# Kernel optimization log

Hardware: AMD Instinct MI355X
Metric: run time of the kernel (lower is better)

## Reference

```python
import jax, jax.numpy as jnp
import numpy as np

B, S, H = 2, 1024, 2048          # batch, seq, hidden
NH, HD = 32, 64                  # heads, head_dim
E, M, K = 8, 1024, 2             # experts, moe_dim, top_k
EPS = 1e-5
ROPE_THETA = 10000.0


def setup_inputs() -> dict:
    key = jax.random.key(0)
    ks = jax.random.split(key, 12)
    sc = lambda *sh: 0.02
    return {
        "hidden_states": jax.random.normal(ks[0], (B, S, H), jnp.float32),
        "w_attn_norm": jnp.ones((H,), jnp.float32),
        "Wq": jax.random.normal(ks[1], (H, H), jnp.float32) * 0.02,
        "Wk": jax.random.normal(ks[2], (H, H), jnp.float32) * 0.02,
        "Wv": jax.random.normal(ks[3], (H, H), jnp.float32) * 0.02,
        "Wo": jax.random.normal(ks[4], (H, H), jnp.float32) * 0.02,
        "w_moe_norm": jnp.ones((H,), jnp.float32),
        "Wr": jax.random.normal(ks[5], (H, E), jnp.float32) * 0.02,
        "Wgate": jax.random.normal(ks[6], (E, H, M), jnp.float32) * 0.02,
        "Wup": jax.random.normal(ks[7], (E, H, M), jnp.float32) * 0.02,
        "Wdown": jax.random.normal(ks[8], (E, M, H), jnp.float32) * 0.02,
    }


def _rmsnorm(x, w):
    return x * jax.lax.rsqrt(jnp.mean(x * x, axis=-1, keepdims=True) + EPS) * w


def _rope_cos_sin(seq_len, dtype):
    inv_freq = 1.0 / (ROPE_THETA ** (jnp.arange(0, HD, 2, dtype=jnp.float32) / HD))
    ang = jnp.arange(seq_len, dtype=jnp.float32)[:, None] * inv_freq[None, :]  # [S, HD/2]
    cos = jnp.concatenate([jnp.cos(ang), jnp.cos(ang)], axis=-1).astype(dtype)  # [S, HD]
    sin = jnp.concatenate([jnp.sin(ang), jnp.sin(ang)], axis=-1).astype(dtype)
    return cos, sin


def _rotate_half(x):
    x1, x2 = jnp.split(x, 2, axis=-1)
    return jnp.concatenate([-x2, x1], axis=-1)


def _attention(x, Wq, Wk, Wv, Wo, mask):
    b, s, _ = x.shape
    def heads(t):  # [b,s,H] -> [b,NH,s,HD]
        return t.reshape(b, s, NH, HD).transpose(0, 2, 1, 3)
    q, k, v = heads(x @ Wq), heads(x @ Wk), heads(x @ Wv)
    cos, sin = _rope_cos_sin(s, x.dtype)
    q = q * cos + _rotate_half(q) * sin
    k = k * cos + _rotate_half(k) * sin
    scores = jnp.einsum("bhqd,bhkd->bhqk", q, k) / jnp.sqrt(jnp.asarray(HD, x.dtype))
    scores = scores + mask  # [1,1,s,s] causal
    attn = jax.nn.softmax(scores, axis=-1)
    out = jnp.einsum("bhqk,bhkd->bhqd", attn, v)
    out = out.transpose(0, 2, 1, 3).reshape(b, s, H)
    return out @ Wo


def _moe(x, Wr, Wgate, Wup, Wdown):
    b, s, _ = x.shape
    xf = x.reshape(b * s, H)  # [T, H]
    logits = xf @ Wr  # [T, E]
    probs = jax.nn.softmax(logits, axis=-1)
    topv, topi = jax.lax.top_k(probs, K)  # [T, K]
    topv = topv / jnp.sum(topv, axis=-1, keepdims=True)
    # combine weights [T, E], zero for unselected experts
    cw = jnp.sum(jax.nn.one_hot(topi, E, dtype=xf.dtype) * topv[..., None], axis=1)
    g = jnp.einsum("th,ehm->etm", xf, Wgate)
    u = jnp.einsum("th,ehm->etm", xf, Wup)
    h = jax.nn.silu(g) * u
    expert_out = jnp.einsum("etm,emh->eth", h, Wdown)  # [E, T, H]
    out = jnp.einsum("eth,te->th", expert_out, cw)
    return out.reshape(b, s, H)


def reference(hidden_states, w_attn_norm, Wq, Wk, Wv, Wo, w_moe_norm, Wr, Wgate, Wup, Wdown):
    b, s, _ = hidden_states.shape
    causal = jnp.triu(jnp.full((s, s), -jnp.inf, hidden_states.dtype), k=1)[None, None]
    residual = hidden_states
    x = _rmsnorm(hidden_states, w_attn_norm)
    x = _attention(x, Wq, Wk, Wv, Wo, causal)
    x = x + residual
    residual = x
    y = _rmsnorm(x, w_moe_norm)
    y = _moe(y, Wr, Wgate, Wup, Wdown)
    return y + residual
```

## Files before the change

kernel.cpp:

```cpp
#include <hip/hip_runtime.h>
#include <hip/hip_bf16.h>
#include <cstdint>

typedef unsigned short u16;
typedef __bf16 bf16x4_t __attribute__((ext_vector_type(4)));
typedef __bf16 bf16x8_t __attribute__((ext_vector_type(8)));
typedef float f32x4_t __attribute__((ext_vector_type(4)));
typedef unsigned short us4_t __attribute__((ext_vector_type(4)));
typedef unsigned short us8_t __attribute__((ext_vector_type(8)));

#define BATCH 2
#define SEQ 1024
#define HID 2048
#define NHEAD 32
#define NEXP 8
#define MDIM 1024
#define T_TOK (BATCH*SEQ)


__device__ __forceinline__ void gload16(const void* g, void* l){
  __builtin_amdgcn_global_load_lds((__attribute__((address_space(1))) void*)(uintptr_t)g,
                                   (__attribute__((address_space(3))) void*)l, 16, 0, 0);
}

__device__ __forceinline__ bf16x8_t ldfsw64(const u16* base, int row, int colbyte){
  const char* p = (const char*)base + row*64;
  int sw = (row & 3) << 4;
  bf16x4_t a = *(const bf16x4_t*)(p + (colbyte ^ sw));
  bf16x4_t b = *(const bf16x4_t*)(p + ((colbyte + 32) ^ sw));
  return __builtin_shufflevector(a, b, 0,1,2,3,4,5,6,7);
}

__device__ __forceinline__ f32x4_t mfma16(bf16x8_t a, bf16x8_t b, f32x4_t c){
  return __builtin_amdgcn_mfma_f32_16x16x32_bf16(a, b, c, 0, 0, 0);
}

__device__ __forceinline__ u16 f2b(float f){
  __hip_bfloat16 h = __float2bfloat16(f);
  return __builtin_bit_cast(u16, h);
}
__device__ __forceinline__ float b2f(u16 b){
  return __builtin_bit_cast(float, (unsigned int)b << 16);
}
__device__ __forceinline__ void split3v(float v, u16& b1, u16& b2, u16& b3){
  b1 = f2b(v); float f1 = b2f(b1);
  float r1 = v - f1;
  b2 = f2b(r1); float f2 = b2f(b2);
  b3 = f2b(r1 - f2);
}



__global__ __launch_bounds__(256)
void convT_fl(const float* __restrict__ in, u16* __restrict__ out, int R, int C)
{
  __shared__ float t[64][65];
  const int KB = C >> 5;
  int bz = blockIdx.z;
  const float* ip = in + (size_t)bz * R * C;
  u16* op = out + (size_t)bz * R * C;
  int r0 = blockIdx.y*64, c0 = blockIdx.x*64;
  int tid = threadIdx.x;
  int lr = tid >> 4;
  int lc = (tid & 15) * 4;
  #pragma unroll
  for (int i = 0; i < 4; i++){
    int r = lr + i*16;
    float4 v = *(const float4*)&ip[(size_t)(r0 + r) * R + c0 + lc];
    t[r][lc] = v.x; t[r][lc+1] = v.y; t[r][lc+2] = v.z; t[r][lc+3] = v.w;
  }
  __syncthreads();
  if (tid < 128){
    int n_l = tid & 63;
    int kb2 = tid >> 6;
    int gn = c0 + n_l;
    int rb = gn >> 7, sub = (gn >> 4) & 7, frn = gn & 15;
    int kb = (r0 >> 5) + kb2;
    size_t fo = (((size_t)(rb*KB + kb)*8 + sub)*64 + frn*4) * 8;
    #pragma unroll
    for (int fg = 0; fg < 4; fg++){
      us8_t w;
      #pragma unroll
      for (int j = 0; j < 4; j++){
        w[j]   = f2b(t[kb2*32 + fg*4 + j][n_l]);
        w[j+4] = f2b(t[kb2*32 + fg*4 + 16 + j][n_l]);
      }
      *(us8_t*)&op[fo + fg*8] = w;
    }
  }
}


__global__ __launch_bounds__(256)
void convT3(const float* __restrict__ in, u16* __restrict__ o1, u16* __restrict__ o2,
            u16* __restrict__ o3)
{
  __shared__ float t[64][65];
  int r0 = blockIdx.y*64, c0 = blockIdx.x*64;
  int tid = threadIdx.x;
  int lr = tid >> 4;
  int lc = (tid & 15) * 4;
  #pragma unroll
  for (int i = 0; i < 4; i++){
    int r = lr + i*16;
    float4 v = *(const float4*)&in[(size_t)(r0 + r) * HID + c0 + lc];
    t[r][lc] = v.x; t[r][lc+1] = v.y; t[r][lc+2] = v.z; t[r][lc+3] = v.w;
  }
  __syncthreads();
  if (tid < 128){
    int n  = tid & 63;
    int kb2 = tid >> 6;
    int gn = c0 + n;
    int nb = gn >> 7, sub = (gn >> 4) & 7, fr = gn & 15;
    int kb = (r0 >> 5) + kb2;
    size_t fo = (((size_t)(nb*64 + kb)*8 + sub)*64 + fr*4) * 8;
    #pragma unroll
    for (int fg = 0; fg < 4; fg++){
      us8_t w1, w2, w3;
      #pragma unroll
      for (int j = 0; j < 4; j++){
        u16 b1, b2, b3;
        split3v(t[kb2*32 + fg*4 + j][n], b1, b2, b3);
        w1[j] = b1; w2[j] = b2; w3[j] = b3;
        split3v(t[kb2*32 + fg*4 + 16 + j][n], b1, b2, b3);
        w1[j+4] = b1; w2[j+4] = b2; w3[j+4] = b3;
      }
      *(us8_t*)&o1[fo + fg*8] = w1;
      *(us8_t*)&o2[fo + fg*8] = w2;
      *(us8_t*)&o3[fo + fg*8] = w3;
    }
  }
}


__global__ __launch_bounds__(256)
void rmsnorm3_k(const float* __restrict__ x, const float* __restrict__ w,
                u16* __restrict__ o1, u16* __restrict__ o2, u16* __restrict__ o3)
{
  int row = blockIdx.x;
  const float* xr = x + (size_t)row * HID;
  int tid = threadIdx.x;
  int kb = tid >> 2, fg = tid & 3;
  int kbase = kb*32 + fg*4;
  float4 a = *(const float4*)(xr + kbase);
  float4 b = *(const float4*)(xr + kbase + 16);
  float ss = a.x*a.x + a.y*a.y + a.z*a.z + a.w*a.w
           + b.x*b.x + b.y*b.y + b.z*b.z + b.w*b.w;
  #pragma unroll
  for (int off = 32; off; off >>= 1) ss += __shfl_down(ss, off);
  __shared__ float red[4];
  if ((tid & 63) == 0) red[tid >> 6] = ss;
  __syncthreads();
  float tot = red[0] + red[1] + red[2] + red[3];
  float rs = (float)(1.0 / sqrt((double)tot * (1.0/2048.0) + 1e-5));
  float4 wa = *(const float4*)(w + kbase);
  float4 wb = *(const float4*)(w + kbase + 16);
  float o[8];
  o[0]=a.x*rs*wa.x; o[1]=a.y*rs*wa.y; o[2]=a.z*rs*wa.z; o[3]=a.w*rs*wa.w;
  o[4]=b.x*rs*wb.x; o[5]=b.y*rs*wb.y; o[6]=b.z*rs*wb.z; o[7]=b.w*rs*wb.w;
  us8_t w1, w2, w3;
  #pragma unroll
  for (int j = 0; j < 8; j++){
    u16 b1, b2, b3; split3v(o[j], b1, b2, b3);
    w1[j] = b1; w2[j] = b2; w3[j] = b3;
  }
  int rb = row >> 7, sub = (row >> 4) & 7, fr = row & 15;
  size_t fo = (((size_t)(rb*64 + kb)*8 + sub)*64 + fr*4 + fg) * 8;
  *(us8_t*)&o1[fo] = w1; *(us8_t*)&o2[fo] = w2; *(us8_t*)&o3[fo] = w3;
}


__global__ __launch_bounds__(256)
void rmsnorm_k(const float* __restrict__ x, const float* __restrict__ w,
               u16* __restrict__ ob, float* __restrict__ of, float* __restrict__ oi)
{
  int row = blockIdx.x;
  const float* xr = x + (size_t)row * HID;
  int base = threadIdx.x * 8;
  float4 a = *(const float4*)(xr + base);
  float4 b = *(const float4*)(xr + base + 4);
  float ss = a.x*a.x + a.y*a.y + a.z*a.z + a.w*a.w
           + b.x*b.x + b.y*b.y + b.z*b.z + b.w*b.w;
  #pragma unroll
  for (int off = 32; off; off >>= 1) ss += __shfl_down(ss, off);
  __shared__ float red[4];
  if ((threadIdx.x & 63) == 0) red[threadIdx.x >> 6] = ss;
  __syncthreads();
  float tot = red[0] + red[1] + red[2] + red[3];
  float rs = (float)(1.0 / sqrt((double)tot * (1.0/2048.0) + 1e-5));
  float4 wa = *(const float4*)(w + base);
  float4 wb = *(const float4*)(w + base + 4);
  float o[8];
  o[0]=a.x*rs*wa.x; o[1]=a.y*rs*wa.y; o[2]=a.z*rs*wa.z; o[3]=a.w*rs*wa.w;
  o[4]=b.x*rs*wb.x; o[5]=b.y*rs*wb.y; o[6]=b.z*rs*wb.z; o[7]=b.w*rs*wb.w;
  us4_t p0, p1;
  p0.x=f2b(o[0]); p0.y=f2b(o[1]); p0.z=f2b(o[2]); p0.w=f2b(o[3]);
  p1.x=f2b(o[4]); p1.y=f2b(o[5]); p1.z=f2b(o[6]); p1.w=f2b(o[7]);
  *(us4_t*)&ob[(size_t)row*HID + base] = p0;
  *(us4_t*)&ob[(size_t)row*HID + base + 4] = p1;
  float* orow = of + (size_t)row*HID + base;
  *(float4*)orow = make_float4(o[0],o[1],o[2],o[3]);
  *(float4*)(orow+4) = make_float4(o[4],o[5],o[6],o[7]);
  float* irow = oi + (size_t)row*HID + base;
  *(float4*)irow = a;
  *(float4*)(irow+4) = b;
}


__global__ void rope_table_k(float* ct, float* st){
  int i = blockIdx.x*256 + threadIdx.x;
  int s = i >> 5, j = i & 31;
  double invf = exp(-(double)j / 32.0 * log(10000.0));
  double ang = (double)s * invf;
  ct[i] = (float)cos(ang);
  st[i] = (float)sin(ang);
}


__global__ __launch_bounds__(256, 2)
void gemm_qkv(const u16* __restrict__ A1, const u16* __restrict__ A2, const u16* __restrict__ A3,
              const u16* __restrict__ Wq1, const u16* __restrict__ Wq2, const u16* __restrict__ Wq3,
              const u16* __restrict__ Wk1, const u16* __restrict__ Wk2, const u16* __restrict__ Wk3,
              const u16* __restrict__ Wv1, const u16* __restrict__ Wv2, const u16* __restrict__ Wv3,
              u16* __restrict__ oq1, u16* __restrict__ oq2, u16* __restrict__ oq3,
              u16* __restrict__ ok1, u16* __restrict__ ok2, u16* __restrict__ ok3,
              float* __restrict__ vf,
              const float* __restrict__ ct, const float* __restrict__ st)
{
  __shared__ u16 As[3][128*32];
  __shared__ u16 Bs[3][128*32];
  const int flat = blockIdx.x + 16*blockIdx.y + 256*blockIdx.z;
  const int logical = (flat & 7) * 96 + (flat >> 3);
  const int z  = logical >> 8;
  const int bm = ((logical >> 4) & 15) * 128;
  const int bn = (logical & 15) * 128;
  const int tid = threadIdx.x;
  const int lane = tid & 63;
  const int wave = tid >> 6;
  const int wr = wave >> 1, wc = wave & 1;
  const int fr = lane & 15, fg = lane >> 4;

  f32x4_t acc[4][4] = {};

  const u16* Ap[3] = {A1, A2, A3};
  const u16* Bp[3];
  if (z == 0)      { Bp[0] = Wq1; Bp[1] = Wq2; Bp[2] = Wq3; }
  else if (z == 1) { Bp[0] = Wk1; Bp[1] = Wk2; Bp[2] = Wk3; }
  else             { Bp[0] = Wv1; Bp[1] = Wv2; Bp[2] = Wv3; }
  const u16* gA[3]; const u16* gB[3];
  #pragma unroll
  for (int t = 0; t < 3; t++){
    gA[t] = Ap[t] + (size_t)(bm >> 7) * 64 * 4096 + tid*8;
    gB[t] = Bp[t] + (size_t)(bn >> 7) * 64 * 4096 + tid*8;
  }

  for (int kb = 0; kb < 64; kb++){
    const size_t o = (size_t)kb * 4096;
    #pragma unroll
    for (int t = 0; t < 3; t++){
      gload16(gA[t] + o,        &As[t][tid*8]);
      gload16(gA[t] + o + 2048, &As[t][2048 + tid*8]);
      gload16(gB[t] + o,        &Bs[t][tid*8]);
      gload16(gB[t] + o + 2048, &Bs[t][2048 + tid*8]);
    }
    __syncthreads();
    bf16x8_t bfv[3][4];
    #pragma unroll
    for (int t = 0; t < 3; t++)
      #pragma unroll
      for (int ni = 0; ni < 4; ni++)
        bfv[t][ni] = *(const bf16x8_t*)&Bs[t][(((wc*4 + ni)*64) + fr*4 + fg)*8];
    #pragma unroll
    for (int mi = 0; mi < 4; mi++){
      const int ao = (((wr*4 + mi)*64) + fr*4 + fg)*8;
      bf16x8_t a1 = *(const bf16x8_t*)&As[0][ao];
      bf16x8_t a2 = *(const bf16x8_t*)&As[1][ao];
      bf16x8_t a3 = *(const bf16x8_t*)&As[2][ao];
      #pragma unroll
      for (int ni = 0; ni < 4; ni++){
        f32x4_t c = acc[mi][ni];
        c = mfma16(a3, bfv[0][ni], c);
        c = mfma16(a2, bfv[1][ni], c);
        c = mfma16(a1, bfv[2][ni], c);
        c = mfma16(a2, bfv[0][ni], c);
        c = mfma16(a1, bfv[1][ni], c);
        c = mfma16(a1, bfv[0][ni], c);
        acc[mi][ni] = c;
      }
    }
    __syncthreads();
  }

  if (z < 2){
    u16* O1 = z ? ok1 : oq1;
    u16* O2 = z ? ok2 : oq2;
    u16* O3 = z ? ok3 : oq3;
    const int h = (bn + wc*64) >> 6;
    #pragma unroll
    for (int mi = 0; mi < 4; mi++)
      #pragma unroll
      for (int r = 0; r < 4; r++){
        int row = bm + wr*64 + mi*16 + fg*4 + r;
        int s = row & (SEQ-1);
        int b = row >> 10;
        int tok = row & 1023;
        int tb = tok >> 4;
        int frk = fg*4 + r;
        size_t sb = (size_t)(b*NHEAD + h) * 65536;
        #pragma unroll
        for (int ni = 0; ni < 2; ni++){
          int dlo = ni*16 + fr;
          float c  = ct[s*32 + dlo];
          float sn = st[s*32 + dlo];
          float xl = acc[mi][ni][r], xh = acc[mi][ni+2][r];
          float ol = xl*c - xh*sn;
          float oh = xh*c + xl*sn;
          size_t a0 = sb + ((size_t)(tb*2 + 0)*64 + frk*4 + (fr>>2))*8 + ni*4 + (fr&3);
          size_t a1 = sb + ((size_t)(tb*2 + 1)*64 + frk*4 + (fr>>2))*8 + ni*4 + (fr&3);
          u16 b1, b2, b3;
          split3v(ol, b1, b2, b3); O1[a0] = b1; O2[a0] = b2; O3[a0] = b3;
          split3v(oh, b1, b2, b3); O1[a1] = b1; O2[a1] = b2; O3[a1] = b3;
        }
      }
  } else {
    #pragma unroll
    for (int mi = 0; mi < 4; mi++)
      #pragma unroll
      for (int ni = 0; ni < 4; ni++)
        #pragma unroll
        for (int r = 0; r < 4; r++){
          int row = bm + wr*64 + mi*16 + fg*4 + r;
          int col = bn + wc*64 + ni*16 + fr;
          vf[(size_t)row * HID + col] = acc[mi][ni][r];
        }
  }
}


__global__ __launch_bounds__(256, 2)
void gemm_o(const u16* __restrict__ A1, const u16* __restrict__ A2, const u16* __restrict__ A3,
            const u16* __restrict__ B1, const u16* __restrict__ B2, const u16* __restrict__ B3,
            float* __restrict__ Cf, const float* __restrict__ Res)
{
  __shared__ u16 As[3][128*32];
  __shared__ u16 Bs[3][64*32];
  const int flat = blockIdx.x + 32*blockIdx.y;
  const int logical = (flat & 7) * 64 + (flat >> 3);
  const int bn = (logical & 31) * 64;
  const int bm = (logical >> 5) * 128;
  const int tid = threadIdx.x;
  const int lane = tid & 63;
  const int wave = tid >> 6;
  const int wr = wave >> 1, wc = wave & 1;
  const int fr = lane & 15, fg = lane >> 4;

  f32x4_t acc[4][2] = {};

  const u16* Ap[3] = {A1, A2, A3};
  const u16* Bp[3] = {B1, B2, B3};
  const u16* gA[3]; const u16* gB[3];
  const int sb0 = (bn >> 4) & 7;
  #pragma unroll
  for (int t = 0; t < 3; t++){
    gA[t] = Ap[t] + (size_t)(bm >> 7) * 64 * 4096 + tid*8;
    gB[t] = Bp[t] + (size_t)(bn >> 7) * 64 * 4096 + sb0*512 + tid*8;
  }

  for (int kb = 0; kb < 64; kb++){
    const size_t o = (size_t)kb * 4096;
    #pragma unroll
    for (int t = 0; t < 3; t++){
      gload16(gA[t] + o,        &As[t][tid*8]);
      gload16(gA[t] + o + 2048, &As[t][2048 + tid*8]);
      gload16(gB[t] + o,        &Bs[t][tid*8]);
    }
    __syncthreads();
    bf16x8_t bfv[3][2];
    #pragma unroll
    for (int t = 0; t < 3; t++)
      #pragma unroll
      for (int nj = 0; nj < 2; nj++)
        bfv[t][nj] = *(const bf16x8_t*)&Bs[t][(((wc*2 + nj)*64) + fr*4 + fg)*8];
    #pragma unroll
    for (int mi = 0; mi < 4; mi++){
      const int ao = (((wr*4 + mi)*64) + fr*4 + fg)*8;
      bf16x8_t a1 = *(const bf16x8_t*)&As[0][ao];
      bf16x8_t a2 = *(const bf16x8_t*)&As[1][ao];
      bf16x8_t a3 = *(const bf16x8_t*)&As[2][ao];
      #pragma unroll
      for (int nj = 0; nj < 2; nj++){
        f32x4_t c = acc[mi][nj];
        c = mfma16(a3, bfv[0][nj], c);
        c = mfma16(a2, bfv[1][nj], c);
        c = mfma16(a1, bfv[2][nj], c);
        c = mfma16(a2, bfv[0][nj], c);
        c = mfma16(a1, bfv[1][nj], c);
        c = mfma16(a1, bfv[0][nj], c);
        acc[mi][nj] = c;
      }
    }
    __syncthreads();
  }

  #pragma unroll
  for (int mi = 0; mi < 4; mi++)
    #pragma unroll
    for (int nj = 0; nj < 2; nj++)
      #pragma unroll
      for (int r = 0; r < 4; r++){
        int row = bm + wr*64 + mi*16 + fg*4 + r;
        int col = bn + wc*32 + nj*16 + fr;
        size_t idx = (size_t)row * HID + col;
        Cf[idx] = acc[mi][nj][r] + Res[idx];
      }
}


__global__ __launch_bounds__(256)
void vtrans3_k(const float* __restrict__ vf, u16* __restrict__ t1, u16* __restrict__ t2,
               u16* __restrict__ t3)
{
  __shared__ float t[64][65];
  int st0 = blockIdx.x * 64;
  int bh = blockIdx.y;
  int b = bh >> 5, h = bh & 31;
  int tid = threadIdx.x;
  #pragma unroll
  for (int i = 0; i < 4; i++){
    int idx = tid + i*256;
    int s = idx >> 4, dc = (idx & 15) * 4;
    float4 v = *(const float4*)&vf[(size_t)(b*SEQ + st0 + s) * HID + h*64 + dc];
    t[dc+0][s] = v.x; t[dc+1][s] = v.y; t[dc+2][s] = v.z; t[dc+3][s] = v.w;
  }
  __syncthreads();
  #pragma unroll
  for (int it = 0; it < 2; it++){
    int rho = tid + it*256;
    int kbv_l = rho >> 8;
    int db    = (rho >> 6) & 3;
    int lane  = rho & 63;
    int d = db*16 + (lane >> 2);
    int fgv = lane & 3;
    us8_t w1, w2, w3;
    #pragma unroll
    for (int j = 0; j < 8; j++){
      int half = j >> 2, e = j & 3;
      int tokl = kbv_l*32 + half*16 + fgv*4 + e;
      u16 b1, b2, b3; split3v(t[d][tokl], b1, b2, b3);
      w1[j] = b1; w2[j] = b2; w3[j] = b3;
    }
    size_t base = (size_t)bh*65536 + ((size_t)(((st0>>5) + kbv_l)*4 + db)*64 + lane)*8;
    *(us8_t*)&t1[base] = w1; *(us8_t*)&t2[base] = w2; *(us8_t*)&t3[base] = w3;
  }
}


__global__ __launch_bounds__(256)
void fattn3_k(const u16* __restrict__ q1, const u16* __restrict__ q2, const u16* __restrict__ q3,
              const u16* __restrict__ k1, const u16* __restrict__ k2, const u16* __restrict__ k3,
              const u16* __restrict__ v1, const u16* __restrict__ v2, const u16* __restrict__ v3,
              u16* __restrict__ ao1, u16* __restrict__ ao2, u16* __restrict__ ao3)
{
  __shared__ u16 Ks[3][4096];
  __shared__ u16 Vs[3][4096];
  __shared__ u16 Ps[2][4][1024];
  const int bh = blockIdx.x, qt = blockIdx.y;
  const int b = bh >> 5, h = bh & 31;
  const int tid = threadIdx.x, lane = tid & 63, wave = tid >> 6;
  const int fr = lane & 15, fg = lane >> 4;
  const size_t hslab = (size_t)bh * 65536;

  bf16x8_t aq[3][2];
  {
    size_t qo = hslab + (size_t)(qt*4 + wave)*1024 + (size_t)(fr*4 + fg)*8;
    aq[0][0] = *(const bf16x8_t*)&q1[qo]; aq[0][1] = *(const bf16x8_t*)&q1[qo + 512];
    aq[1][0] = *(const bf16x8_t*)&q2[qo]; aq[1][1] = *(const bf16x8_t*)&q2[qo + 512];
    aq[2][0] = *(const bf16x8_t*)&q3[qo]; aq[2][1] = *(const bf16x8_t*)&q3[qo + 512];
  }

  f32x4_t oacc[4] = {};
  float m_r[4], l_r[4];
  #pragma unroll
  for (int r = 0; r < 4; r++){ m_r[r] = -1e30f; l_r[r] = 0.f; }

  const u16* kp[3] = { k1 + hslab, k2 + hslab, k3 + hslab };
  const u16* vp[3] = { v1 + hslab, v2 + hslab, v3 + hslab };

  for (int kt = 0; kt <= qt; kt++){
    const size_t o = (size_t)kt * 4096;
    #pragma unroll
    for (int t = 0; t < 3; t++){
      gload16(kp[t] + o + tid*8,        &Ks[t][tid*8]);
      gload16(kp[t] + o + 2048 + tid*8, &Ks[t][2048 + tid*8]);
      gload16(vp[t] + o + tid*8,        &Vs[t][tid*8]);
      gload16(vp[t] + o + 2048 + tid*8, &Vs[t][2048 + tid*8]);
    }
    __syncthreads();

    f32x4_t sc[4] = {};
    #pragma unroll
    for (int nf = 0; nf < 4; nf++)
      #pragma unroll
      for (int ks = 0; ks < 2; ks++){
        const int ko = ((nf*2 + ks)*64 + fr*4 + fg)*8;
        bf16x8_t bk0 = *(const bf16x8_t*)&Ks[0][ko];
        bf16x8_t bk1 = *(const bf16x8_t*)&Ks[1][ko];
        bf16x8_t bk2 = *(const bf16x8_t*)&Ks[2][ko];
        sc[nf] = mfma16(aq[2][ks], bk0, sc[nf]);
        sc[nf] = mfma16(aq[1][ks], bk1, sc[nf]);
        sc[nf] = mfma16(aq[0][ks], bk2, sc[nf]);
        sc[nf] = mfma16(aq[1][ks], bk0, sc[nf]);
        sc[nf] = mfma16(aq[0][ks], bk1, sc[nf]);
        sc[nf] = mfma16(aq[0][ks], bk0, sc[nf]);
      }

    float nm[4] = {-1e30f,-1e30f,-1e30f,-1e30f};
    #pragma unroll
    for (int nf = 0; nf < 4; nf++)
      #pragma unroll
      for (int r = 0; r < 4; r++){
        float v = sc[nf][r] * 0.125f;
        if (kt == qt && nf*16 + fr > wave*16 + fg*4 + r) v = -1e30f;
        sc[nf][r] = v;
        nm[r] = fmaxf(nm[r], v);
      }
    #pragma unroll
    for (int r = 0; r < 4; r++)
      #pragma unroll
      for (int msk = 8; msk; msk >>= 1) nm[r] = fmaxf(nm[r], __shfl_xor(nm[r], msk));

    #pragma unroll
    for (int r = 0; r < 4; r++){
      float mn = fmaxf(m_r[r], nm[r]);
      float f = __expf(m_r[r] - mn);
      m_r[r] = mn;
      float rsum = 0.f;
      #pragma unroll
      for (int nf = 0; nf < 4; nf++){
        float pv = __expf(sc[nf][r] - mn);
        sc[nf][r] = pv;
        rsum += pv;
      }
      #pragma unroll
      for (int msk = 8; msk; msk >>= 1) rsum += __shfl_xor(rsum, msk);
      l_r[r] = l_r[r]*f + rsum;
      #pragma unroll
      for (int df = 0; df < 4; df++) oacc[df][r] *= f;
    }

    #pragma unroll
    for (int nf = 0; nf < 4; nf++)
      #pragma unroll
      for (int r = 0; r < 4; r++){
        float pv = sc[nf][r];
        u16 b1 = f2b(pv);
        float f1 = b2f(b1);
        u16 b2 = f2b(pv - f1);
        int pa = ((nf>>1)*64 + (fg*4 + r)*4 + (fr>>2))*8 + (nf&1)*4 + (fr&3);
        Ps[0][wave][pa] = b1;
        Ps[1][wave][pa] = b2;
      }

    #pragma unroll
    for (int ks = 0; ks < 2; ks++){
      bf16x8_t pa0 = *(const bf16x8_t*)&Ps[0][wave][(ks*64 + fr*4 + fg)*8];
      bf16x8_t pa1 = *(const bf16x8_t*)&Ps[1][wave][(ks*64 + fr*4 + fg)*8];
      #pragma unroll
      for (int df = 0; df < 4; df++){
        const int vo = ((ks*4 + df)*64 + fr*4 + fg)*8;
        bf16x8_t bv0 = *(const bf16x8_t*)&Vs[0][vo];
        bf16x8_t bv1 = *(const bf16x8_t*)&Vs[1][vo];
        bf16x8_t bv2 = *(const bf16x8_t*)&Vs[2][vo];
        oacc[df] = mfma16(pa0, bv2, oacc[df]);
        oacc[df] = mfma16(pa1, bv1, oacc[df]);
        oacc[df] = mfma16(pa1, bv0, oacc[df]);
        oacc[df] = mfma16(pa0, bv1, oacc[df]);
        oacc[df] = mfma16(pa0, bv0, oacc[df]);
      }
    }
    __syncthreads();
  }

  #pragma unroll
  for (int r = 0; r < 4; r++){
    float inv = 1.f / l_r[r];
    int orow = b*SEQ + qt*64 + wave*16 + fg*4 + r;
    int rb = orow >> 7, sub = (orow >> 4) & 7, frA = orow & 15;
    #pragma unroll
    for (int df = 0; df < 4; df++){
      float val = oacc[df][r] * inv;
      int kb = h*2 + (df >> 1);
      size_t addr = ((((size_t)rb*64 + kb)*8 + sub)*64 + frA*4 + (fr>>2))*8 + (df&1)*4 + (fr&3);
      u16 b1, b2, b3; split3v(val, b1, b2, b3);
      ao1[addr] = b1; ao2[addr] = b2; ao3[addr] = b3;
    }
  }
}


__global__ __launch_bounds__(64)
void router_scatter_k(const float* __restrict__ yn, const float* __restrict__ Wr,
                      int* __restrict__ tok_list, float* __restrict__ w_list,
                      int* __restrict__ cur){
  int row = blockIdx.x;
  int lane = threadIdx.x;
  const float* xr = yn + (size_t)row * HID;
  double acc[8] = {};
  for (int j = lane; j < HID; j += 64){
    double xv = (double)xr[j];
    const float* wr = Wr + (size_t)j*8;
    float4 w0 = *(const float4*)wr;
    float4 w1 = *(const float4*)(wr + 4);
    acc[0] += xv*w0.x; acc[1] += xv*w0.y; acc[2] += xv*w0.z; acc[3] += xv*w0.w;
    acc[4] += xv*w1.x; acc[5] += xv*w1.y; acc[6] += xv*w1.z; acc[7] += xv*w1.w;
  }
  #pragma unroll
  for (int e = 0; e < 8; e++)
    #pragma unroll
    for (int off = 32; off; off >>= 1) acc[e] += __shfl_down(acc[e], off);
  if (lane == 0){
    double mx = acc[0];
    #pragma unroll
    for (int e = 1; e < 8; e++) mx = fmax(mx, acc[e]);
    double p[8];
    #pragma unroll
    for (int e = 0; e < 8; e++) p[e] = exp(acc[e] - mx);
    int i1 = 0;
    #pragma unroll
    for (int e = 1; e < 8; e++) if (p[e] > p[i1]) i1 = e;
    int i2 = (i1 == 0) ? 1 : 0;
    #pragma unroll
    for (int e = 0; e < 8; e++) if (e != i1 && p[e] > p[i2]) i2 = e;
    double s2 = p[i1] + p[i2];
    int pos1 = atomicAdd(&cur[i1], 1);
    tok_list[i1*T_TOK + pos1] = row;
    w_list[i1*T_TOK + pos1] = (float)(p[i1] / s2);
    int pos2 = atomicAdd(&cur[i2], 1);
    tok_list[i2*T_TOK + pos2] = row;
    w_list[i2*T_TOK + pos2] = (float)(p[i2] / s2);
  }
}

__global__ __launch_bounds__(128)
void pad_k(const int* __restrict__ cur, int* __restrict__ tok_list,
           float* __restrict__ w_list, int* __restrict__ cnt_pad){
  int e = blockIdx.x;
  int c = cur[e];
  int cp = (c + 127) & ~127;
  for (int i = c + threadIdx.x; i < cp; i += 128){
    tok_list[e*T_TOK + i] = 0;
    w_list[e*T_TOK + i] = 0.f;
  }
  if (threadIdx.x == 0) cnt_pad[e] = cp;
}


__global__ __launch_bounds__(256, 2)
void gemm_gateup_sp(const u16* __restrict__ A, const u16* __restrict__ WgT, const u16* __restrict__ WuT,
                    const int* __restrict__ tok_list, const float* __restrict__ w_list,
                    const int* __restrict__ cnt_pad, u16* __restrict__ Hb)
{
  const int e = blockIdx.z;
  const int bm = blockIdx.y * 128;
  if (bm >= cnt_pad[e]) return;
  __shared__ u16 As[128*32];
  __shared__ u16 Bg[64*32];
  __shared__ u16 Bu[64*32];
  const int tid = threadIdx.x;
  const int lane = tid & 63;
  const int wave = tid >> 6;
  const int wr = wave >> 1, wc = wave & 1;
  const int fr = lane & 15, fg = lane >> 4;
  const int bn = blockIdx.x * 64;

  f32x4_t ag[4][2] = {}, au[4][2] = {};

  const int srow = tid >> 2, skb = (tid & 3) ^ (srow & 3);
  const int tok0 = tok_list[e*T_TOK + bm + srow];
  const int tok1 = tok_list[e*T_TOK + bm + srow + 64];
  const u16* ga0 = A + (size_t)tok0 * HID + skb * 8;
  const u16* ga1 = A + (size_t)tok1 * HID + skb * 8;
  const int sub0 = (bn >> 4) & 7;
  const u16* gg = WgT + (size_t)e*MDIM*HID + ((size_t)(bn>>7)*512 + sub0)*512 + tid*8;
  const u16* gu = WuT + (size_t)e*MDIM*HID + ((size_t)(bn>>7)*512 + sub0)*512 + tid*8;

  for (int kb = 0; kb < 64; kb++){
    gload16(ga0 + kb*32, &As[tid*8]);
    gload16(ga1 + kb*32, &As[2048 + tid*8]);
    gload16(gg + (size_t)kb*4096, &Bg[tid*8]);
    gload16(gu + (size_t)kb*4096, &Bu[tid*8]);
    __syncthreads();
    bf16x8_t af[4], bg[2], bu[2];
    #pragma unroll
    for (int i = 0; i < 4; i++) af[i] = ldfsw64(As, wr*64 + i*16 + fr, fg*8);
    #pragma unroll
    for (int j = 0; j < 2; j++){
      bg[j] = *(const bf16x8_t*)&Bg[((wc*2 + j)*64 + fr*4 + fg)*8];
      bu[j] = *(const bf16x8_t*)&Bu[((wc*2 + j)*64 + fr*4 + fg)*8];
    }
    #pragma unroll
    for (int mi = 0; mi < 4; mi++)
      #pragma unroll
      for (int nj = 0; nj < 2; nj++){
        ag[mi][nj] = mfma16(af[mi], bg[nj], ag[mi][nj]);
        au[mi][nj] = mfma16(af[mi], bu[nj], au[mi][nj]);
      }
    __syncthreads();
  }

  #pragma unroll
  for (int mi = 0; mi < 4; mi++)
    #pragma unroll
    for (int nj = 0; nj < 2; nj++)
      #pragma unroll
      for (int r = 0; r < 4; r++){
        int pos = bm + wr*64 + mi*16 + fg*4 + r;
        int col = bn + wc*32 + nj*16 + fr;
        float g = ag[mi][nj][r], u = au[mi][nj][r];
        float h = g / (1.0f + __expf(-g)) * u * w_list[e*T_TOK + pos];
        Hb[((size_t)e*T_TOK + pos)*MDIM + col] = f2b(h);
      }
}


__global__ __launch_bounds__(256, 2)
void gemm_down_sp(const u16* __restrict__ Hb, const u16* __restrict__ WdT,
                  const int* __restrict__ tok_list, const int* __restrict__ cnt_pad,
                  float* __restrict__ Out)
{
  const int e = blockIdx.z;
  const int bm = blockIdx.y * 128;
  if (bm >= cnt_pad[e]) return;
  __shared__ u16 As[128*32];
  __shared__ u16 Bs[128*32];
  const int tid = threadIdx.x;
  const int lane = tid & 63;
  const int wave = tid >> 6;
  const int wr = wave >> 1, wc = wave & 1;
  const int fr = lane & 15, fg = lane >> 4;
  const int bn = blockIdx.x * 128;
  const int srow = tid >> 2, skb = (tid & 3) ^ (srow & 3);

  f32x4_t acc[4][4] = {};

  const u16* A  = Hb  + (size_t)e * T_TOK * MDIM;
  const u16* ga0 = A + (size_t)(bm + srow) * MDIM + skb * 8;
  const u16* gB = WdT + (size_t)e*HID*MDIM + (size_t)(bn>>7)*131072 + tid*8;
  for (int kb = 0; kb < 32; kb++){
    gload16(ga0 + kb*32, &As[tid*8]);
    gload16(ga0 + (size_t)64*MDIM + kb*32, &As[2048 + tid*8]);
    gload16(gB + (size_t)kb*4096,        &Bs[tid*8]);
    gload16(gB + (size_t)kb*4096 + 2048, &Bs[2048 + tid*8]);
    __syncthreads();
    bf16x8_t af[4], bfv[4];
    #pragma unroll
    for (int i = 0; i < 4; i++) af[i]  = ldfsw64(As, wr*64 + i*16 + fr, fg*8);
    #pragma unroll
    for (int i = 0; i < 4; i++) bfv[i] = *(const bf16x8_t*)&Bs[((wc*4 + i)*64 + fr*4 + fg)*8];
    #pragma unroll
    for (int mi = 0; mi < 4; mi++)
      #pragma unroll
      for (int ni = 0; ni < 4; ni++)
        acc[mi][ni] = mfma16(af[mi], bfv[ni], acc[mi][ni]);
    __syncthreads();
  }

  #pragma unroll
  for (int mi = 0; mi < 4; mi++)
    #pragma unroll
    for (int r = 0; r < 4; r++){
      int pos = bm + wr*64 + mi*16 + fg*4 + r;
      int tok = tok_list[e*T_TOK + pos];
      #pragma unroll
      for (int ni = 0; ni < 4; ni++){
        int col = bn + wc*64 + ni*16 + fr;
        atomicAdd(&Out[(size_t)tok * HID + col], acc[mi][ni][r]);
      }
    }
}


extern "C" void kernel_launch(void* const* d_in, const int* in_sizes, int n_in,
                              void* d_out, int out_size, void* d_ws, size_t ws_size,
                              hipStream_t stream)
{
  const float* hs     = (const float*)d_in[0];
  const float* w_attn = (const float*)d_in[1];
  const float* Wq = (const float*)d_in[2];
  const float* Wk = (const float*)d_in[3];
  const float* Wv = (const float*)d_in[4];
  const float* Wo = (const float*)d_in[5];
  const float* w_moe = (const float*)d_in[6];
  const float* Wr = (const float*)d_in[7];
  const float* Wg = (const float*)d_in[8];
  const float* Wu = (const float*)d_in[9];
  const float* Wd = (const float*)d_in[10];
  float* out = (float*)d_out;
  (void)in_sizes; (void)n_in; (void)out_size; (void)ws_size;

  char* ws = (char*)d_ws;
  const size_t MB = 1024*1024;
  char* R0 = ws;
  char* R1 = ws + 96*MB;
  char* R2 = ws + 120*MB;
  char* R3 = ws + 144*MB;
  char* R4 = ws + 168*MB;
  char* R5 = ws + 184*MB;
  char* RS = ws + 208*MB;

  const size_t WSLB = (size_t)HID*HID;
  u16* W0 = (u16*)R0;
  u16 *Wq1 = W0,          *Wq2 = W0 + WSLB,    *Wq3 = W0 + 2*WSLB;
  u16 *Wk1 = W0 + 3*WSLB, *Wk2 = W0 + 4*WSLB,  *Wk3 = W0 + 5*WSLB;
  u16 *Wv1 = W0 + 6*WSLB, *Wv2 = W0 + 7*WSLB,  *Wv3 = W0 + 8*WSLB;
  u16 *Wo1 = W0 + 9*WSLB, *Wo2 = W0 + 10*WSLB, *Wo3 = W0 + 11*WSLB;
  const size_t TSLB = (size_t)T_TOK*HID;
  u16 *xn1 = (u16*)R1, *xn2 = (u16*)R1 + TSLB, *xn3 = (u16*)R1 + 2*TSLB;
  u16 *q1  = (u16*)R2, *q2  = (u16*)R2 + TSLB, *q3  = (u16*)R2 + 2*TSLB;
  u16 *k1  = (u16*)R3, *k2  = (u16*)R3 + TSLB, *k3  = (u16*)R3 + 2*TSLB;
  u16 *vt1 = xn1, *vt2 = xn2, *vt3 = xn3;
  float* vf  = (float*)R4;
  float* x1  = (float*)R4;
  u16 *ao1 = (u16*)R5, *ao2 = (u16*)R5 + TSLB, *ao3 = (u16*)R5 + 2*TSLB;
  u16* WgT = (u16*)R0;
  u16* WuT = (u16*)R0 + (size_t)NEXP*MDIM*HID;
  u16* WdT = (u16*)R0 + 2*(size_t)NEXP*MDIM*HID;
  u16* ynb = (u16*)R1;
  float* yn = (float*)(R1 + 8*MB);
  u16* hb  = (u16*)R2;
  int*   tok_list = (int*)RS;
  float* w_list   = (float*)(RS + 64*1024);
  int*   cur      = (int*)(RS + 128*1024);
  int*   cnt_pad  = (int*)(RS + 132*1024);
  float* ct   = (float*)(RS + 256*1024);
  float* stab = (float*)(RS + 384*1024);

  dim3 blk256(256), gMoE(16,16,8);

  rope_table_k<<<dim3(SEQ*32/256), blk256, 0, stream>>>(ct, stab);
  convT3<<<dim3(HID/64, HID/64), blk256, 0, stream>>>(Wq, Wq1, Wq2, Wq3);
  convT3<<<dim3(HID/64, HID/64), blk256, 0, stream>>>(Wk, Wk1, Wk2, Wk3);
  convT3<<<dim3(HID/64, HID/64), blk256, 0, stream>>>(Wv, Wv1, Wv2, Wv3);
  convT3<<<dim3(HID/64, HID/64), blk256, 0, stream>>>(Wo, Wo1, Wo2, Wo3);

  rmsnorm3_k<<<dim3(T_TOK), blk256, 0, stream>>>(hs, w_attn, xn1, xn2, xn3);

  gemm_qkv<<<dim3(16,16,3), blk256, 0, stream>>>(xn1,xn2,xn3,
      Wq1,Wq2,Wq3, Wk1,Wk2,Wk3, Wv1,Wv2,Wv3,
      q1,q2,q3, k1,k2,k3, vf, ct, stab);

  vtrans3_k<<<dim3(SEQ/64, BATCH*NHEAD), blk256, 0, stream>>>(vf, vt1, vt2, vt3);

  fattn3_k<<<dim3(BATCH*NHEAD, SEQ/64), blk256, 0, stream>>>(q1,q2,q3, k1,k2,k3,
      vt1,vt2,vt3, ao1,ao2,ao3);

  gemm_o<<<dim3(32,16), blk256, 0, stream>>>(ao1,ao2,ao3, Wo1,Wo2,Wo3, x1, hs);

  convT_fl<<<dim3(MDIM/64, HID/64, NEXP), blk256, 0, stream>>>(Wg, WgT, MDIM, HID);
  convT_fl<<<dim3(MDIM/64, HID/64, NEXP), blk256, 0, stream>>>(Wu, WuT, MDIM, HID);
  convT_fl<<<dim3(HID/64, MDIM/64, NEXP), blk256, 0, stream>>>(Wd, WdT, HID, MDIM);

  rmsnorm_k<<<dim3(T_TOK), blk256, 0, stream>>>(x1, w_moe, ynb, yn, out);

  hipMemsetAsync(cur, 0, NEXP*sizeof(int), stream);
  router_scatter_k<<<dim3(T_TOK), dim3(64), 0, stream>>>(yn, Wr, tok_list, w_list, cur);
  pad_k<<<dim3(NEXP), dim3(128), 0, stream>>>(cur, tok_list, w_list, cnt_pad);

  gemm_gateup_sp<<<gMoE, blk256, 0, stream>>>(ynb, WgT, WuT, tok_list, w_list, cnt_pad, hb);
  gemm_down_sp<<<gMoE, blk256, 0, stream>>>(hb, WdT, tok_list, cnt_pad, out);
}
```

Baseline: 843.8 us.

## Load B operands directly from global into registers, dropping LDS staging

In the QKV, O-projection, MoE gate/up and down GEMMs and the flash-attention kernel, the pre-fragmented weight/K/V tiles are now read straight from global memory into registers in MFMA fragment layout instead of being staged through shared memory. This frees LDS so the launch bounds are raised to allow three blocks per CU, and the attention kernel loses its per-tile barriers. The trade-off is that each wave now fetches B fragments independently, so waves sharing a column slice read the same data twice and L2/global traffic rises. Load latency is also no longer hidden behind an LDS barrier.

```diff
diff --git a/kernel.cpp b/kernel.cpp
--- a/kernel.cpp
+++ b/kernel.cpp
@@ -217,7 +217,7 @@
 }
 
 
-__global__ __launch_bounds__(256, 2)
+__global__ __launch_bounds__(256, 3)
 void gemm_qkv(const u16* __restrict__ A1, const u16* __restrict__ A2, const u16* __restrict__ A3,
               const u16* __restrict__ Wq1, const u16* __restrict__ Wq2, const u16* __restrict__ Wq3,
               const u16* __restrict__ Wk1, const u16* __restrict__ Wk2, const u16* __restrict__ Wk3,
@@ -228,7 +228,6 @@
               const float* __restrict__ ct, const float* __restrict__ st)
 {
   __shared__ u16 As[3][128*32];
-  __shared__ u16 Bs[3][128*32];
   const int flat = blockIdx.x + 16*blockIdx.y + 256*blockIdx.z;
   const int logical = (flat & 7) * 96 + (flat >> 3);
   const int z  = logical >> 8;
@@ -247,11 +246,11 @@
   if (z == 0)      { Bp[0] = Wq1; Bp[1] = Wq2; Bp[2] = Wq3; }
   else if (z == 1) { Bp[0] = Wk1; Bp[1] = Wk2; Bp[2] = Wk3; }
   else             { Bp[0] = Wv1; Bp[1] = Wv2; Bp[2] = Wv3; }
-  const u16* gA[3]; const u16* gB[3];
+  const u16* gA[3]; const u16* gBf[3];
   #pragma unroll
   for (int t = 0; t < 3; t++){
-    gA[t] = Ap[t] + (size_t)(bm >> 7) * 64 * 4096 + tid*8;
-    gB[t] = Bp[t] + (size_t)(bn >> 7) * 64 * 4096 + tid*8;
+    gA[t]  = Ap[t] + (size_t)(bm >> 7) * 262144 + tid*8;
+    gBf[t] = Bp[t] + (size_t)(bn >> 7) * 262144 + ((wc*4)*64 + fr*4 + fg)*8;
   }
 
   for (int kb = 0; kb < 64; kb++){
@@ -260,16 +259,14 @@
     for (int t = 0; t < 3; t++){
       gload16(gA[t] + o,        &As[t][tid*8]);
       gload16(gA[t] + o + 2048, &As[t][2048 + tid*8]);
-      gload16(gB[t] + o,        &Bs[t][tid*8]);
-      gload16(gB[t] + o + 2048, &Bs[t][2048 + tid*8]);
-    }
+    }
+    bf16x8_t bfv[3][4];
+    #pragma unroll
+    for (int t = 0; t < 3; t++)
+      #pragma unroll
+      for (int ni = 0; ni < 4; ni++)
+        bfv[t][ni] = *(const bf16x8_t*)(gBf[t] + o + ni*512);
     __syncthreads();
-    bf16x8_t bfv[3][4];
-    #pragma unroll
-    for (int t = 0; t < 3; t++)
-      #pragma unroll
-      for (int ni = 0; ni < 4; ni++)
-        bfv[t][ni] = *(const bf16x8_t*)&Bs[t][(((wc*4 + ni)*64) + fr*4 + fg)*8];
     #pragma unroll
     for (int mi = 0; mi < 4; mi++){
       const int ao = (((wr*4 + mi)*64) + fr*4 + fg)*8;
@@ -343,7 +340,6 @@
             float* __restrict__ Cf, const float* __restrict__ Res)
 {
   __shared__ u16 As[3][128*32];
-  __shared__ u16 Bs[3][64*32];
   const int flat = blockIdx.x + 32*blockIdx.y;
   const int logical = (flat & 7) * 64 + (flat >> 3);
   const int bn = (logical & 31) * 64;
@@ -358,12 +354,12 @@
 
   const u16* Ap[3] = {A1, A2, A3};
   const u16* Bp[3] = {B1, B2, B3};
-  const u16* gA[3]; const u16* gB[3];
+  const u16* gA[3]; const u16* gBf[3];
   const int sb0 = (bn >> 4) & 7;
   #pragma unroll
   for (int t = 0; t < 3; t++){
-    gA[t] = Ap[t] + (size_t)(bm >> 7) * 64 * 4096 + tid*8;
-    gB[t] = Bp[t] + (size_t)(bn >> 7) * 64 * 4096 + sb0*512 + tid*8;
+    gA[t]  = Ap[t] + (size_t)(bm >> 7) * 262144 + tid*8;
+    gBf[t] = Bp[t] + (size_t)(bn >> 7) * 262144 + (size_t)(sb0 + wc*2)*512 + (fr*4 + fg)*8;
   }
 
   for (int kb = 0; kb < 64; kb++){
@@ -372,15 +368,14 @@
     for (int t = 0; t < 3; t++){
       gload16(gA[t] + o,        &As[t][tid*8]);
       gload16(gA[t] + o + 2048, &As[t][2048 + tid*8]);
-      gload16(gB[t] + o,        &Bs[t][tid*8]);
-    }
+    }
+    bf16x8_t bfv[3][2];
+    #pragma unroll
+    for (int t = 0; t < 3; t++)
+      #pragma unroll
+      for (int nj = 0; nj < 2; nj++)
+        bfv[t][nj] = *(const bf16x8_t*)(gBf[t] + o + nj*512);
     __syncthreads();
-    bf16x8_t bfv[3][2];
-    #pragma unroll
-    for (int t = 0; t < 3; t++)
-      #pragma unroll
-      for (int nj = 0; nj < 2; nj++)
-        bfv[t][nj] = *(const bf16x8_t*)&Bs[t][(((wc*2 + nj)*64) + fr*4 + fg)*8];
     #pragma unroll
     for (int mi = 0; mi < 4; mi++){
       const int ao = (((wr*4 + mi)*64) + fr*4 + fg)*8;
@@ -455,14 +450,12 @@
 }
 
 
-__global__ __launch_bounds__(256)
+__global__ __launch_bounds__(256, 3)
 void fattn3_k(const u16* __restrict__ q1, const u16* __restrict__ q2, const u16* __restrict__ q3,
               const u16* __restrict__ k1, const u16* __restrict__ k2, const u16* __restrict__ k3,
               const u16* __restrict__ v1, const u16* __restrict__ v2, const u16* __restrict__ v3,
               u16* __restrict__ ao1, u16* __restrict__ ao2, u16* __restrict__ ao3)
 {
-  __shared__ u16 Ks[3][4096];
-  __shared__ u16 Vs[3][4096];
   __shared__ u16 Ps[2][4][1024];
   const int bh = blockIdx.x, qt = blockIdx.y;
   const int b = bh >> 5, h = bh & 31;
@@ -483,29 +476,22 @@
   #pragma unroll
   for (int r = 0; r < 4; r++){ m_r[r] = -1e30f; l_r[r] = 0.f; }
 
-  const u16* kp[3] = { k1 + hslab, k2 + hslab, k3 + hslab };
-  const u16* vp[3] = { v1 + hslab, v2 + hslab, v3 + hslab };
+  const int fo = (fr*4 + fg)*8;
+  const u16* kf[3] = { k1 + hslab + fo, k2 + hslab + fo, k3 + hslab + fo };
+  const u16* vfp[3] = { v1 + hslab + fo, v2 + hslab + fo, v3 + hslab + fo };
 
   for (int kt = 0; kt <= qt; kt++){
     const size_t o = (size_t)kt * 4096;
-    #pragma unroll
-    for (int t = 0; t < 3; t++){
-      gload16(kp[t] + o + tid*8,        &Ks[t][tid*8]);
-      gload16(kp[t] + o + 2048 + tid*8, &Ks[t][2048 + tid*8]);
-      gload16(vp[t] + o + tid*8,        &Vs[t][tid*8]);
-      gload16(vp[t] + o + 2048 + tid*8, &Vs[t][2048 + tid*8]);
-    }
-    __syncthreads();
 
     f32x4_t sc[4] = {};
     #pragma unroll
     for (int nf = 0; nf < 4; nf++)
       #pragma unroll
       for (int ks = 0; ks < 2; ks++){
-        const int ko = ((nf*2 + ks)*64 + fr*4 + fg)*8;
-        bf16x8_t bk0 = *(const bf16x8_t*)&Ks[0][ko];
-        bf16x8_t bk1 = *(const bf16x8_t*)&Ks[1][ko];
-        bf16x8_t bk2 = *(const bf16x8_t*)&Ks[2][ko];
+        const size_t ko = o + (nf*2 + ks)*512;
+        bf16x8_t bk0 = *(const bf16x8_t*)(kf[0] + ko);
+        bf16x8_t bk1 = *(const bf16x8_t*)(kf[1] + ko);
+        bf16x8_t bk2 = *(const bf16x8_t*)(kf[2] + ko);
         sc[nf] = mfma16(aq[2][ks], bk0, sc[nf]);
         sc[nf] = mfma16(aq[1][ks], bk1, sc[nf]);
         sc[nf] = mfma16(aq[0][ks], bk2, sc[nf]);
@@ -567,10 +553,10 @@
       bf16x8_t pa1 = *(const bf16x8_t*)&Ps[1][wave][(ks*64 + fr*4 + fg)*8];
       #pragma unroll
       for (int df = 0; df < 4; df++){
-        const int vo = ((ks*4 + df)*64 + fr*4 + fg)*8;
-        bf16x8_t bv0 = *(const bf16x8_t*)&Vs[0][vo];
-        bf16x8_t bv1 = *(const bf16x8_t*)&Vs[1][vo];
-        bf16x8_t bv2 = *(const bf16x8_t*)&Vs[2][vo];
+        const size_t vo = o + (ks*4 + df)*512;
+        bf16x8_t bv0 = *(const bf16x8_t*)(vfp[0] + vo);
+        bf16x8_t bv1 = *(const bf16x8_t*)(vfp[1] + vo);
+        bf16x8_t bv2 = *(const bf16x8_t*)(vfp[2] + vo);
         oacc[df] = mfma16(pa0, bv2, oacc[df]);
         oacc[df] = mfma16(pa1, bv1, oacc[df]);
         oacc[df] = mfma16(pa1, bv0, oacc[df]);
@@ -578,7 +564,6 @@
         oacc[df] = mfma16(pa0, bv0, oacc[df]);
       }
     }
-    __syncthreads();
   }
 
   #pragma unroll
@@ -664,8 +649,6 @@
   const int bm = blockIdx.y * 128;
   if (bm >= cnt_pad[e]) return;
   __shared__ u16 As[128*32];
-  __shared__ u16 Bg[64*32];
-  __shared__ u16 Bu[64*32];
   const int tid = threadIdx.x;
   const int lane = tid & 63;
   const int wave = tid >> 6;
@@ -681,23 +664,24 @@
   const u16* ga0 = A + (size_t)tok0 * HID + skb * 8;
   const u16* ga1 = A + (size_t)tok1 * HID + skb * 8;
   const int sub0 = (bn >> 4) & 7;
-  const u16* gg = WgT + (size_t)e*MDIM*HID + ((size_t)(bn>>7)*512 + sub0)*512 + tid*8;
-  const u16* gu = WuT + (size_t)e*MDIM*HID + ((size_t)(bn>>7)*512 + sub0)*512 + tid*8;
+  const size_t bb = (size_t)e*MDIM*HID + (size_t)(bn>>7)*262144 + (size_t)(sub0 + wc*2)*512 + (fr*4 + fg)*8;
+  const u16* ggf = WgT + bb;
+  const u16* guf = WuT + bb;
 
   for (int kb = 0; kb < 64; kb++){
     gload16(ga0 + kb*32, &As[tid*8]);
     gload16(ga1 + kb*32, &As[2048 + tid*8]);
-    gload16(gg + (size_t)kb*4096, &Bg[tid*8]);
-    gload16(gu + (size_t)kb*4096, &Bu[tid*8]);
+    const size_t o = (size_t)kb*4096;
+    bf16x8_t bg[2], bu[2];
+    #pragma unroll
+    for (int j = 0; j < 2; j++){
+      bg[j] = *(const bf16x8_t*)(ggf + o + j*512);
+      bu[j] = *(const bf16x8_t*)(guf + o + j*512);
+    }
     __syncthreads();
-    bf16x8_t af[4], bg[2], bu[2];
+    bf16x8_t af[4];
     #pragma unroll
     for (int i = 0; i < 4; i++) af[i] = ldfsw64(As, wr*64 + i*16 + fr, fg*8);
-    #pragma unroll
-    for (int j = 0; j < 2; j++){
-      bg[j] = *(const bf16x8_t*)&Bg[((wc*2 + j)*64 + fr*4 + fg)*8];
-      bu[j] = *(const bf16x8_t*)&Bu[((wc*2 + j)*64 + fr*4 + fg)*8];
-    }
     #pragma unroll
     for (int mi = 0; mi < 4; mi++)
       #pragma unroll
@@ -732,7 +716,6 @@
   const int bm = blockIdx.y * 128;
   if (bm >= cnt_pad[e]) return;
   __shared__ u16 As[128*32];
-  __shared__ u16 Bs[128*32];
   const int tid = threadIdx.x;
   const int lane = tid & 63;
   const int wave = tid >> 6;
@@ -745,18 +728,18 @@
 
   const u16* A  = Hb  + (size_t)e * T_TOK * MDIM;
   const u16* ga0 = A + (size_t)(bm + srow) * MDIM + skb * 8;
-  const u16* gB = WdT + (size_t)e*HID*MDIM + (size_t)(bn>>7)*131072 + tid*8;
+  const u16* gBf = WdT + (size_t)e*HID*MDIM + (size_t)(bn>>7)*131072 + (size_t)(wc*4)*512 + (fr*4 + fg)*8;
   for (int kb = 0; kb < 32; kb++){
     gload16(ga0 + kb*32, &As[tid*8]);
     gload16(ga0 + (size_t)64*MDIM + kb*32, &As[2048 + tid*8]);
-    gload16(gB + (size_t)kb*4096,        &Bs[tid*8]);
-    gload16(gB + (size_t)kb*4096 + 2048, &Bs[2048 + tid*8]);
+    const size_t o = (size_t)kb*4096;
+    bf16x8_t bfv[4];
+    #pragma unroll
+    for (int i = 0; i < 4; i++) bfv[i] = *(const bf16x8_t*)(gBf + o + i*512);
     __syncthreads();
-    bf16x8_t af[4], bfv[4];
-    #pragma unroll
-    for (int i = 0; i < 4; i++) af[i]  = ldfsw64(As, wr*64 + i*16 + fr, fg*8);
-    #pragma unroll
-    for (int i = 0; i < 4; i++) bfv[i] = *(const bf16x8_t*)&Bs[((wc*4 + i)*64 + fr*4 + fg)*8];
+    bf16x8_t af[4];
+    #pragma unroll
+    for (int i = 0; i < 4; i++) af[i] = ldfsw64(As, wr*64 + i*16 + fr, fg*8);
     #pragma unroll
     for (int mi = 0; mi < 4; mi++)
       #pragma unroll
```

Result: slower. 897.1 us (+6.3%).

## Fuse V transpose and bf16 split into QKV GEMM epilogue, remap attention grid

Applied to the files above, without the earlier changes.

The QKV GEMM epilogue now splits V into three bf16 parts and writes them straight into the transposed tiled layout that flash attention reads. This removes the fp32 V round trip through memory and the separate vtrans3_k launch. The attention grid index is also remapped so consecutive workgroups are spread across XCDs by head/q-tile, and workspace regions are reorganized so vt no longer aliases xn. The epilogue stores are 8-byte scattered writes, which may coalesce less well than the old transpose kernel's writes.

```diff
diff --git a/kernel.cpp b/kernel.cpp
--- a/kernel.cpp
+++ b/kernel.cpp
@@ -224,7 +224,7 @@
               const u16* __restrict__ Wv1, const u16* __restrict__ Wv2, const u16* __restrict__ Wv3,
               u16* __restrict__ oq1, u16* __restrict__ oq2, u16* __restrict__ oq3,
               u16* __restrict__ ok1, u16* __restrict__ ok2, u16* __restrict__ ok3,
-              float* __restrict__ vf,
+              u16* __restrict__ vt1, u16* __restrict__ vt2, u16* __restrict__ vt3,
               const float* __restrict__ ct, const float* __restrict__ st)
 {
   __shared__ u16 As[3][128*32];
@@ -250,8 +250,8 @@
   const u16* gA[3]; const u16* gB[3];
   #pragma unroll
   for (int t = 0; t < 3; t++){
-    gA[t] = Ap[t] + (size_t)(bm >> 7) * 64 * 4096 + tid*8;
-    gB[t] = Bp[t] + (size_t)(bn >> 7) * 64 * 4096 + tid*8;
+    gA[t] = Ap[t] + (size_t)(bm >> 7) * 262144 + tid*8;
+    gB[t] = Bp[t] + (size_t)(bn >> 7) * 262144 + tid*8;
   }
 
   for (int kb = 0; kb < 64; kb++){
@@ -323,16 +323,26 @@
         }
       }
   } else {
-    #pragma unroll
-    for (int mi = 0; mi < 4; mi++)
-      #pragma unroll
-      for (int ni = 0; ni < 4; ni++)
+    const int h = (bn + wc*64) >> 6;
+    const int b = bm >> 10;
+    const size_t sb = (size_t)(b*NHEAD + h) * 65536;
+    const int tokb = (bm & 1023) + wr*64;
+    #pragma unroll
+    for (int mi = 0; mi < 4; mi++){
+      const int kbv = (tokb + mi*16) >> 5;
+      const int el = (mi & 1) * 4;
+      #pragma unroll
+      for (int ni = 0; ni < 4; ni++){
+        us4_t v1, v2, v3;
         #pragma unroll
         for (int r = 0; r < 4; r++){
-          int row = bm + wr*64 + mi*16 + fg*4 + r;
-          int col = bn + wc*64 + ni*16 + fr;
-          vf[(size_t)row * HID + col] = acc[mi][ni][r];
+          u16 b1, b2, b3; split3v(acc[mi][ni][r], b1, b2, b3);
+          v1[r] = b1; v2[r] = b2; v3[r] = b3;
         }
+        size_t a = sb + ((size_t)(kbv*4 + ni)*64 + fr*4 + fg)*8 + el;
+        *(us4_t*)&vt1[a] = v1; *(us4_t*)&vt2[a] = v2; *(us4_t*)&vt3[a] = v3;
+      }
+    }
   }
 }
 
@@ -362,8 +372,8 @@
   const int sb0 = (bn >> 4) & 7;
   #pragma unroll
   for (int t = 0; t < 3; t++){
-    gA[t] = Ap[t] + (size_t)(bm >> 7) * 64 * 4096 + tid*8;
-    gB[t] = Bp[t] + (size_t)(bn >> 7) * 64 * 4096 + sb0*512 + tid*8;
+    gA[t] = Ap[t] + (size_t)(bm >> 7) * 262144 + tid*8;
+    gB[t] = Bp[t] + (size_t)(bn >> 7) * 262144 + sb0*512 + tid*8;
   }
 
   for (int kb = 0; kb < 64; kb++){
@@ -417,45 +427,6 @@
 
 
 __global__ __launch_bounds__(256)
-void vtrans3_k(const float* __restrict__ vf, u16* __restrict__ t1, u16* __restrict__ t2,
-               u16* __restrict__ t3)
-{
-  __shared__ float t[64][65];
-  int st0 = blockIdx.x * 64;
-  int bh = blockIdx.y;
-  int b = bh >> 5, h = bh & 31;
-  int tid = threadIdx.x;
-  #pragma unroll
-  for (int i = 0; i < 4; i++){
-    int idx = tid + i*256;
-    int s = idx >> 4, dc = (idx & 15) * 4;
-    float4 v = *(const float4*)&vf[(size_t)(b*SEQ + st0 + s) * HID + h*64 + dc];
-    t[dc+0][s] = v.x; t[dc+1][s] = v.y; t[dc+2][s] = v.z; t[dc+3][s] = v.w;
-  }
-  __syncthreads();
-  #pragma unroll
-  for (int it = 0; it < 2; it++){
-    int rho = tid + it*256;
-    int kbv_l = rho >> 8;
-    int db    = (rho >> 6) & 3;
-    int lane  = rho & 63;
-    int d = db*16 + (lane >> 2);
-    int fgv = lane & 3;
-    us8_t w1, w2, w3;
-    #pragma unroll
-    for (int j = 0; j < 8; j++){
-      int half = j >> 2, e = j & 3;
-      int tokl = kbv_l*32 + half*16 + fgv*4 + e;
-      u16 b1, b2, b3; split3v(t[d][tokl], b1, b2, b3);
-      w1[j] = b1; w2[j] = b2; w3[j] = b3;
-    }
-    size_t base = (size_t)bh*65536 + ((size_t)(((st0>>5) + kbv_l)*4 + db)*64 + lane)*8;
-    *(us8_t*)&t1[base] = w1; *(us8_t*)&t2[base] = w2; *(us8_t*)&t3[base] = w3;
-  }
-}
-
-
-__global__ __launch_bounds__(256)
 void fattn3_k(const u16* __restrict__ q1, const u16* __restrict__ q2, const u16* __restrict__ q3,
               const u16* __restrict__ k1, const u16* __restrict__ k2, const u16* __restrict__ k3,
               const u16* __restrict__ v1, const u16* __restrict__ v2, const u16* __restrict__ v3,
@@ -464,7 +435,9 @@
   __shared__ u16 Ks[3][4096];
   __shared__ u16 Vs[3][4096];
   __shared__ u16 Ps[2][4][1024];
-  const int bh = blockIdx.x, qt = blockIdx.y;
+  const int flat = blockIdx.x + 64*blockIdx.y;
+  const int logical = (flat & 7) * 128 + (flat >> 3);
+  const int bh = logical >> 4, qt = logical & 15;
   const int b = bh >> 5, h = bh & 31;
   const int tid = threadIdx.x, lane = tid & 63, wave = tid >> 6;
   const int fr = lane & 15, fg = lane >> 4;
@@ -804,9 +777,9 @@
   char* R1 = ws + 96*MB;
   char* R2 = ws + 120*MB;
   char* R3 = ws + 144*MB;
-  char* R4 = ws + 168*MB;
-  char* R5 = ws + 184*MB;
-  char* RS = ws + 208*MB;
+  char* R5 = ws + 168*MB;
+  char* R6 = ws + 192*MB;
+  char* RS = ws + 216*MB;
 
   const size_t WSLB = (size_t)HID*HID;
   u16* W0 = (u16*)R0;
@@ -818,10 +791,9 @@
   u16 *xn1 = (u16*)R1, *xn2 = (u16*)R1 + TSLB, *xn3 = (u16*)R1 + 2*TSLB;
   u16 *q1  = (u16*)R2, *q2  = (u16*)R2 + TSLB, *q3  = (u16*)R2 + 2*TSLB;
   u16 *k1  = (u16*)R3, *k2  = (u16*)R3 + TSLB, *k3  = (u16*)R3 + 2*TSLB;
-  u16 *vt1 = xn1, *vt2 = xn2, *vt3 = xn3;
-  float* vf  = (float*)R4;
-  float* x1  = (float*)R4;
   u16 *ao1 = (u16*)R5, *ao2 = (u16*)R5 + TSLB, *ao3 = (u16*)R5 + 2*TSLB;
+  u16 *vt1 = (u16*)R6, *vt2 = (u16*)R6 + TSLB, *vt3 = (u16*)R6 + 2*TSLB;
+  float* x1  = (float*)R6;
   u16* WgT = (u16*)R0;
   u16* WuT = (u16*)R0 + (size_t)NEXP*MDIM*HID;
   u16* WdT = (u16*)R0 + 2*(size_t)NEXP*MDIM*HID;
@@ -847,11 +819,9 @@
 
   gemm_qkv<<<dim3(16,16,3), blk256, 0, stream>>>(xn1,xn2,xn3,
       Wq1,Wq2,Wq3, Wk1,Wk2,Wk3, Wv1,Wv2,Wv3,
-      q1,q2,q3, k1,k2,k3, vf, ct, stab);
-
-  vtrans3_k<<<dim3(SEQ/64, BATCH*NHEAD), blk256, 0, stream>>>(vf, vt1, vt2, vt3);
-
-  fattn3_k<<<dim3(BATCH*NHEAD, SEQ/64), blk256, 0, stream>>>(q1,q2,q3, k1,k2,k3,
+      q1,q2,q3, k1,k2,k3, vt1,vt2,vt3, ct, stab);
+
+  fattn3_k<<<dim3(64, 16), blk256, 0, stream>>>(q1,q2,q3, k1,k2,k3,
       vt1,vt2,vt3, ao1,ao2,ao3);
 
   gemm_o<<<dim3(32,16), blk256, 0, stream>>>(ao1,ao2,ao3, Wo1,Wo2,Wo3, x1, hs);
```

Measured after the change: 855.0 us. About the same (+1.3%).
